# Optimization experiments

Measured on AMD Instinct MI355X. Metric: run time of the kernel, lower is better.

The kernel has to match this reference:

```python
import jax, jax.numpy as jnp
import numpy as np

N = 131072      # number of nodes / samples
IN_DIM = 128    # input_dim
H = 128         # hidden_dim
OUT_DIM = 10    # output_dim


def setup_inputs() -> dict:
    key = jax.random.key(0)
    ks = jax.random.split(key, 20)
    s = 0.05
    def rn(k, shape):
        return jax.random.normal(k, shape, jnp.float32) * s
    return {
        "x": jax.random.normal(ks[0], (N, IN_DIM), jnp.float32),
        # GRU layer 1 (seq_len=1, h0=0 => weight_hh contributes nothing; only b_hh matters)
        "w_ih_f1": rn(ks[1], (3 * H, IN_DIM)), "b_ih_f1": rn(ks[2], (3 * H,)), "b_hh_f1": rn(ks[3], (3 * H,)),
        "w_ih_b1": rn(ks[4], (3 * H, IN_DIM)), "b_ih_b1": rn(ks[5], (3 * H,)), "b_hh_b1": rn(ks[6], (3 * H,)),
        # GRU layer 2 (input 2H)
        "w_ih_f2": rn(ks[7], (3 * H, 2 * H)), "b_ih_f2": rn(ks[8], (3 * H,)), "b_hh_f2": rn(ks[9], (3 * H,)),
        "w_ih_b2": rn(ks[10], (3 * H, 2 * H)), "b_ih_b2": rn(ks[11], (3 * H,)), "b_hh_b2": rn(ks[12], (3 * H,)),
        # GCNConv layers
        "w_g1": rn(ks[13], (2 * H, 128)), "b_g1": rn(ks[14], (128,)),
        "w_g2": rn(ks[15], (128, 64)), "b_g2": rn(ks[16], (64,)),
        # final fc
        "w_fc": rn(ks[17], (64, OUT_DIM)), "b_fc": rn(ks[18], (OUT_DIM,)),
    }


def _gru_cell_zero(x, w_ih, b_ih, b_hh):
    # PyTorch GRU cell with h_prev = 0: h' = (1 - z) * n_gate
    gi = x @ w_ih.T + b_ih                    # [n, 3H]
    ir, iz, inn = jnp.split(gi, 3, axis=-1)
    hr, hz, hn = jnp.split(b_hh, 3)
    r = jax.nn.sigmoid(ir + hr)
    z = jax.nn.sigmoid(iz + hz)
    ng = jnp.tanh(inn + r * hn)
    return (1.0 - z) * ng


def _gcn(x, w, b, sources, targets, n):
    # PyG GCNConv: D^{-1/2}(A+I)D^{-1/2} X W + b, self-loops already in edge lists
    xw = x @ w                                 # [n, out]
    deg = jax.ops.segment_sum(jnp.ones(sources.shape[0], x.dtype), targets, num_segments=n)
    dinv = jax.lax.rsqrt(deg)
    norm = dinv[sources] * dinv[targets]       # [E]
    msg = norm[:, None] * xw[sources]          # gather
    return jax.ops.segment_sum(msg, targets, num_segments=n) + b  # scatter-add


def reference(x, w_ih_f1, b_ih_f1, b_hh_f1, w_ih_b1, b_ih_b1, b_hh_b1,
              w_ih_f2, b_ih_f2, b_hh_f2, w_ih_b2, b_ih_b2, b_hh_b2,
              w_g1, b_g1, w_g2, b_g2, w_fc, b_fc):
    n = x.shape[0]
    # seq_len = 1 => bidirectional GRU output is [fwd_cell(x); bwd_cell(x)]
    h1 = jnp.concatenate([_gru_cell_zero(x, w_ih_f1, b_ih_f1, b_hh_f1),
                          _gru_cell_zero(x, w_ih_b1, b_ih_b1, b_hh_b1)], axis=-1)
    h2 = jnp.concatenate([_gru_cell_zero(h1, w_ih_f2, b_ih_f2, b_hh_f2),
                          _gru_cell_zero(h1, w_ih_b2, b_ih_b2, b_hh_b2)], axis=-1)
    # chain graph, both directions, plus self loops (GCNConv adds them)
    src = jnp.arange(n - 1)
    dst = jnp.arange(1, n)
    ar = jnp.arange(n)
    sources = jnp.concatenate([src, dst, ar])
    targets = jnp.concatenate([dst, src, ar])
    g1 = _gcn(h2, w_g1, b_g1, sources, targets, n)   # dropout is identity in eval
    g2 = _gcn(g1, w_g2, b_g2, sources, targets, n)
    return g2 @ w_fc + b_fc
```

## Files before the change

### kernel.cpp

```cpp
#include <hip/hip_runtime.h>
#include <stdint.h>

#define N_NODES 131072
#define HDIM 128

typedef __bf16 bf16x8 __attribute__((ext_vector_type(8)));
typedef float f32x4 __attribute__((ext_vector_type(4)));
typedef unsigned short ushort_t;

__device__ __forceinline__ ushort_t f2bf(float f) {
    union { float f; uint32_t i; } v; v.f = f;
    uint32_t i = v.i;
    return (ushort_t)((i + 0x7FFFu + ((i >> 16) & 1u)) >> 16);
}

__device__ __forceinline__ void gll16(const ushort_t* g, ushort_t* l) {
    __builtin_amdgcn_global_load_lds(
        (const __attribute__((address_space(1))) uint32_t*)g,
        (__attribute__((address_space(3))) uint32_t*)l, 16, 0, 0);
}

__device__ __forceinline__ bf16x8 ldsw(const ushort_t* base, int R, int g) {
    return *(const bf16x8*)&base[R * 64 + (((g - R) & 7) << 3)];
}

__device__ __forceinline__ float fsig(float x) {
    return __builtin_amdgcn_rcpf(1.0f + __expf(-x));
}
__device__ __forceinline__ float ftanh(float y) {
    float yc = fminf(fmaxf(y, -15.0f), 15.0f);
    float e = __expf(2.0f * yc);
    return (e - 1.0f) * __builtin_amdgcn_rcpf(e + 1.0f);
}

template<int NC>
__device__ __forceinline__ void swz(int b, int& m, int& c) {
    int mhi = b / (8 * NC);
    int rem = b - mhi * (8 * NC);
    c = rem >> 3;
    m = mhi * 8 + (rem & 7);
}

__global__ __launch_bounds__(256) void prep_all(
    const float* __restrict__ w_f1, const float* __restrict__ w_b1,
    const float* __restrict__ w_f2, const float* __restrict__ w_b2,
    ushort_t* __restrict__ PWF1, ushort_t* __restrict__ PWB1,
    ushort_t* __restrict__ PWF2, ushort_t* __restrict__ PWB2,
    const float* __restrict__ w_g1, const float* __restrict__ b_g1,
    const float* __restrict__ w_g2, const float* __restrict__ b_g2,
    const float* __restrict__ w_fc, const float* __restrict__ b_fc,
    ushort_t* __restrict__ M16, float* __restrict__ cc)
{
    __shared__ float wfc_s[640];
    __shared__ float T1[128][10];
    const int t = threadIdx.x;

    if (blockIdx.x < 1152) {
        int idx = blockIdx.x * 256 + t;
        if (idx < 49152) {
            PWF1[idx] = f2bf(w_f1[idx]);
        } else if (idx < 98304) {
            int j = idx - 49152;  PWB1[j] = f2bf(w_b1[j]);
        } else if (idx < 196608) {
            int j = idx - 98304;  PWF2[j] = f2bf(w_f2[j]);
        } else if (idx < 294912) {
            int j = idx - 196608; PWB2[j] = f2bf(w_b2[j]);
        }
        return;
    }

    for (int i = t; i < 640; i += 256) wfc_s[i] = w_fc[i];
    __syncthreads();
    if (t < 128) {
        float s[10];
        #pragma unroll
        for (int j = 0; j < 10; ++j) s[j] = 0.0f;
        const float4* row = (const float4*)(w_g2 + t * 64);
        #pragma unroll
        for (int k4 = 0; k4 < 16; ++k4) {
            float4 v = row[k4];
            #pragma unroll
            for (int j = 0; j < 10; ++j)
                s[j] += v.x * wfc_s[(k4 * 4 + 0) * 10 + j] + v.y * wfc_s[(k4 * 4 + 1) * 10 + j]
                      + v.z * wfc_s[(k4 * 4 + 2) * 10 + j] + v.w * wfc_s[(k4 * 4 + 3) * 10 + j];
        }
        #pragma unroll
        for (int j = 0; j < 10; ++j) T1[t][j] = s[j];
    }
    __syncthreads();
    float m[10];
    #pragma unroll
    for (int j = 0; j < 10; ++j) m[j] = 0.0f;
    const float4* row1 = (const float4*)(w_g1 + t * 128);
    #pragma unroll 4
    for (int k4 = 0; k4 < 32; ++k4) {
        float4 v = row1[k4];
        #pragma unroll
        for (int j = 0; j < 10; ++j)
            m[j] += v.x * T1[k4 * 4 + 0][j] + v.y * T1[k4 * 4 + 1][j]
                  + v.z * T1[k4 * 4 + 2][j] + v.w * T1[k4 * 4 + 3][j];
    }
    #pragma unroll
    for (int j = 0; j < 16; ++j)
        M16[j * 256 + t] = (j < 10) ? f2bf(m[j]) : (ushort_t)0;
    if (t < 10) {
        float s1 = 0.0f;
        for (int k2 = 0; k2 < 128; ++k2) s1 += b_g1[k2] * T1[k2][t];
        cc[t] = s1;
        float s2 = 0.0f;
        for (int k3 = 0; k3 < 64; ++k3) s2 += b_g2[k3] * wfc_s[k3 * 10 + t];
        cc[16 + t] = s2 + b_fc[t];
    }
}

__global__ __launch_bounds__(512, 4) void gru_l1(
    const float* __restrict__ X,
    const ushort_t* __restrict__ Wf,
    const ushort_t* __restrict__ Wb,
    const float* __restrict__ bi_f, const float* __restrict__ bh_f,
    const float* __restrict__ bi_b, const float* __restrict__ bh_b,
    ushort_t* __restrict__ Hout)
{
    __shared__ ushort_t As[2 * 8192];
    __shared__ ushort_t Bs[96 * 64];
    const int tid = threadIdx.x;
    const int m0 = blockIdx.x * 128;
    const int wv = tid >> 6, lane = tid & 63;
    const int lr = lane & 15, lq = lane >> 4;

    #pragma unroll
    for (int p = 0; p < 4; ++p) {
        int ci = p * 512 + tid;
        int reg = ci >> 10, w = ci & 1023, row = w >> 3, slot = w & 7;
        int g = (slot + row) & 7;
        const float* src = X + (size_t)(m0 + row) * 128 + reg * 64 + g * 8;
        float4 f0 = ((const float4*)src)[0];
        float4 f1 = ((const float4*)src)[1];
        bf16x8 t8;
        t8[0] = (__bf16)f0.x; t8[1] = (__bf16)f0.y; t8[2] = (__bf16)f0.z; t8[3] = (__bf16)f0.w;
        t8[4] = (__bf16)f1.x; t8[5] = (__bf16)f1.y; t8[6] = (__bf16)f1.z; t8[7] = (__bf16)f1.w;
        *(bf16x8*)&As[ci * 8] = t8;
    }
    __syncthreads();

    for (int jc = 0; jc < 8; ++jc) {
        const int dir = jc >> 2;
        const int j0 = (jc & 3) * 32;
        const ushort_t* W = dir ? Wb : Wf;
        const float* b_ih = dir ? bi_b : bi_f;
        const float* b_hh = dir ? bh_b : bh_f;
        const int coloff = dir << 7;

        f32x4 acc[3][2];
        #pragma unroll
        for (int g = 0; g < 3; ++g)
            #pragma unroll
            for (int ct = 0; ct < 2; ++ct)
                #pragma unroll
                for (int e = 0; e < 4; ++e) acc[g][ct][e] = 0.0f;

        for (int t = 0; t < 2; ++t) {
            {
                int ci = tid;
                int r96 = ci >> 3, slot = ci & 7, g = (slot + r96) & 7;
                int wr = ((r96 >> 5) << 7) + j0 + (r96 & 31);
                gll16(W + (size_t)wr * 128 + t * 64 + g * 8, &Bs[ci * 8]);
                if (tid < 256) {
                    int ci2 = 512 + tid;
                    int r2 = ci2 >> 3, s2 = ci2 & 7, g2 = (s2 + r2) & 7;
                    int wr2 = ((r2 >> 5) << 7) + j0 + (r2 & 31);
                    gll16(W + (size_t)wr2 * 128 + t * 64 + g2 * 8, &Bs[ci2 * 8]);
                }
            }
            __syncthreads();
            #pragma unroll
            for (int kk = 0; kk < 64; kk += 32) {
                const int g8 = (kk >> 3) + lq;
                bf16x8 a0 = ldsw(&As[t * 8192], wv * 16 + lr, g8);
                #pragma unroll
                for (int g = 0; g < 3; ++g) {
                    #pragma unroll
                    for (int ct = 0; ct < 2; ++ct) {
                        bf16x8 b = ldsw(Bs, g * 32 + ct * 16 + lr, g8);
                        acc[g][ct] = __builtin_amdgcn_mfma_f32_16x16x32_bf16(a0, b, acc[g][ct], 0, 0, 0);
                    }
                }
            }
            __syncthreads();
        }

        #pragma unroll
        for (int ct = 0; ct < 2; ++ct) {
            const int j = j0 + ct * 16 + lr;
            const float br  = b_ih[j] + b_hh[j];
            const float bz  = b_ih[HDIM + j] + b_hh[HDIM + j];
            const float bn  = b_ih[2 * HDIM + j];
            const float bhn = b_hh[2 * HDIM + j];
            #pragma unroll
            for (int r = 0; r < 4; ++r) {
                const int row = m0 + wv * 16 + lq * 4 + r;
                float rg = fsig(acc[0][ct][r] + br);
                float zg = fsig(acc[1][ct][r] + bz);
                float ng = ftanh(acc[2][ct][r] + bn + rg * bhn);
                ((__bf16*)Hout)[(size_t)row * 256 + coloff + j] = (__bf16)((1.0f - zg) * ng);
            }
        }
    }
}

__global__ __launch_bounds__(256, 5) void gru_l2(
    const ushort_t* __restrict__ A,
    const ushort_t* __restrict__ Wf,
    const ushort_t* __restrict__ Wb,
    const float* __restrict__ bi_f, const float* __restrict__ bh_f,
    const float* __restrict__ bi_b, const float* __restrict__ bh_b,
    const ushort_t* __restrict__ M16,
    float* __restrict__ Zp)
{
    __shared__ ushort_t As[128 * 64];
    __shared__ ushort_t Bs[96 * 64];
    const int tid = threadIdx.x;
    int mt, comb;
    swz<8>(blockIdx.x, mt, comb);
    const int m0 = mt * 128;
    const int dir = comb >> 2;
    const int j0 = (comb & 3) * 32;
    const ushort_t* W = dir ? Wb : Wf;
    const float* b_ih = dir ? bi_b : bi_f;
    const float* b_hh = dir ? bh_b : bh_f;
    const int coloff = dir << 7;

    const int wv = tid >> 6, lane = tid & 63;
    const int lr = lane & 15, lq = lane >> 4;
    const int tr = tid >> 3, tc = tid & 7;
    const int sc = ((tr + tc) & 7) << 3;

    f32x4 acc[3][2][2];
    #pragma unroll
    for (int g = 0; g < 3; ++g)
        #pragma unroll
        for (int rt = 0; rt < 2; ++rt)
            #pragma unroll
            for (int ct = 0; ct < 2; ++ct)
                #pragma unroll
                for (int e = 0; e < 4; ++e) acc[g][rt][ct][e] = 0.0f;

    for (int t = 0; t < 4; ++t) {
        const int k0 = t * 64;
        const ushort_t* ga = A + (size_t)(m0 + tr) * 256 + k0 + sc;
        #pragma unroll
        for (int i = 0; i < 4; ++i)
            gll16(ga + (size_t)i * 32 * 256, &As[(i * 256 + tid) * 8]);
        #pragma unroll
        for (int i = 0; i < 3; ++i) {
            int wr = (i << 7) + j0 + tr;
            gll16(W + (size_t)wr * 256 + k0 + sc, &Bs[(i * 256 + tid) * 8]);
        }
        __syncthreads();
        #pragma unroll
        for (int kk = 0; kk < 64; kk += 32) {
            const int g8 = (kk >> 3) + lq;
            bf16x8 a0 = ldsw(As, wv * 32 + lr, g8);
            bf16x8 a1 = ldsw(As, wv * 32 + 16 + lr, g8);
            #pragma unroll
            for (int g = 0; g < 3; ++g) {
                #pragma unroll
                for (int ct = 0; ct < 2; ++ct) {
                    bf16x8 b = ldsw(Bs, g * 32 + ct * 16 + lr, g8);
                    acc[g][0][ct] = __builtin_amdgcn_mfma_f32_16x16x32_bf16(a0, b, acc[g][0][ct], 0, 0, 0);
                    acc[g][1][ct] = __builtin_amdgcn_mfma_f32_16x16x32_bf16(a1, b, acc[g][1][ct], 0, 0, 0);
                }
            }
        }
        __syncthreads();
    }

    const bf16x8 mb = *(const bf16x8*)&M16[lr * 256 + coloff + j0 + lq * 8];

    ushort_t* hs = &As[wv * 1280];
    #pragma unroll
    for (int ct = 0; ct < 2; ++ct) {
        const int j = j0 + ct * 16 + lr;
        const float br  = b_ih[j] + b_hh[j];
        const float bz  = b_ih[HDIM + j] + b_hh[HDIM + j];
        const float bn  = b_ih[2 * HDIM + j];
        const float bhn = b_hh[2 * HDIM + j];
        #pragma unroll
        for (int rt = 0; rt < 2; ++rt) {
            #pragma unroll
            for (int r = 0; r < 4; ++r) {
                const int lrow = rt * 16 + lq * 4 + r;
                float rg = fsig(acc[0][rt][ct][r] + br);
                float zg = fsig(acc[1][rt][ct][r] + bz);
                float ng = ftanh(acc[2][rt][ct][r] + bn + rg * bhn);
                ((__bf16*)hs)[lrow * 40 + ct * 16 + lr] = (__bf16)((1.0f - zg) * ng);
            }
        }
    }
    __syncthreads();

    bf16x8 ha0 = *(const bf16x8*)&hs[lr * 40 + lq * 8];
    bf16x8 ha1 = *(const bf16x8*)&hs[(16 + lr) * 40 + lq * 8];
    f32x4 z0, z1;
    #pragma unroll
    for (int e = 0; e < 4; ++e) { z0[e] = 0.0f; z1[e] = 0.0f; }
    z0 = __builtin_amdgcn_mfma_f32_16x16x32_bf16(ha0, mb, z0, 0, 0, 0);
    z1 = __builtin_amdgcn_mfma_f32_16x16x32_bf16(ha1, mb, z1, 0, 0, 0);

    if (lr < 10) {
        float* zslice = Zp + (size_t)comb * ((size_t)N_NODES * 10);
        #pragma unroll
        for (int r = 0; r < 4; ++r) {
            zslice[(size_t)(m0 + wv * 32 + lq * 4 + r) * 10 + lr] = z0[r];
            zslice[(size_t)(m0 + wv * 32 + 16 + lq * 4 + r) * 10 + lr] = z1[r];
        }
    }
}

__device__ __forceinline__ float dcoef(int i) {
    return (i == 0 || i == N_NODES - 1) ? 0.70710678118654752f : 0.57735026918962576f;
}
__global__ __launch_bounds__(256) void stz(
    const float* __restrict__ Zp, float* __restrict__ out,
    const float* __restrict__ cc)
{
    __shared__ __align__(16) float zl[2600];
    const int tid = threadIdx.x;
    const int n0 = blockIdx.x * 256;
    const bool edge = (blockIdx.x == 0) || (blockIdx.x == gridDim.x - 1);

    if (!edge) {
        const size_t base4 = ((size_t)n0 * 10 - 20) >> 2;
        const float4* Z4 = (const float4*)Zp;
        for (int i4 = tid; i4 < 650; i4 += 256) {
            float4 a = Z4[base4 + i4];
            #pragma unroll
            for (int s = 1; s < 8; ++s) {
                float4 b = Z4[(size_t)s * ((size_t)N_NODES * 10 / 4) + base4 + i4];
                a.x += b.x; a.y += b.y; a.z += b.z; a.w += b.w;
            }
            ((float4*)zl)[i4] = a;
        }
    } else {
        for (int i = tid; i < 2600; i += 256) {
            int nl = i / 10;
            int c = i - nl * 10;
            int n = n0 - 2 + nl;
            float v = 0.0f;
            if (n >= 0 && n < N_NODES) {
                size_t b = (size_t)n * 10 + c;
                #pragma unroll
                for (int s = 0; s < 8; ++s)
                    v += Zp[(size_t)s * ((size_t)N_NODES * 10) + b];
            }
            zl[i] = v;
        }
    }
    __syncthreads();

    const int i = n0 + tid;
    const float d_i = dcoef(i);
    float dsum = d_i;
    if (i - 1 >= 0) dsum += dcoef(i - 1);
    if (i + 1 < N_NODES) dsum += dcoef(i + 1);

    #pragma unroll
    for (int c = 0; c < 10; ++c) {
        float accv = 0.0f;
        #pragma unroll
        for (int oj = -1; oj <= 1; ++oj) {
            int j = i + oj;
            if (j < 0 || j >= N_NODES) continue;
            float dj = dcoef(j);
            float wj = 0.0f;
            #pragma unroll
            for (int ok = -1; ok <= 1; ++ok) {
                int k = j + ok;
                wj += dcoef(k) * zl[(tid + 2 + oj + ok) * 10 + c];
            }
            accv += dj * dj * wj;
        }
        out[(size_t)i * 10 + c] = d_i * accv + d_i * dsum * cc[c] + cc[16 + c];
    }
}

extern "C" void kernel_launch(void* const* d_in, const int* in_sizes, int n_in,
                              void* d_out, int out_size, void* d_ws, size_t ws_size,
                              hipStream_t stream) {
    const float* x     = (const float*)d_in[0];
    const float* w_f1  = (const float*)d_in[1];
    const float* bi_f1 = (const float*)d_in[2];
    const float* bh_f1 = (const float*)d_in[3];
    const float* w_b1  = (const float*)d_in[4];
    const float* bi_b1 = (const float*)d_in[5];
    const float* bh_b1 = (const float*)d_in[6];
    const float* w_f2  = (const float*)d_in[7];
    const float* bi_f2 = (const float*)d_in[8];
    const float* bh_f2 = (const float*)d_in[9];
    const float* w_b2  = (const float*)d_in[10];
    const float* bi_b2 = (const float*)d_in[11];
    const float* bh_b2 = (const float*)d_in[12];
    const float* w_g1  = (const float*)d_in[13];
    const float* b_g1  = (const float*)d_in[14];
    const float* w_g2  = (const float*)d_in[15];
    const float* b_g2  = (const float*)d_in[16];
    const float* w_fc  = (const float*)d_in[17];
    const float* b_fc  = (const float*)d_in[18];

    char* ws = (char*)d_ws;
    ushort_t* h1   = (ushort_t*)(ws);
    float*    Zp   = (float*)(ws + 67108864);
    ushort_t* PWF1 = (ushort_t*)(ws + 134217728);
    ushort_t* PWB1 = PWF1 + 49152;
    ushort_t* PWF2 = PWB1 + 49152;
    ushort_t* PWB2 = PWF2 + 98304;
    ushort_t* M16  = PWB2 + 98304;
    float*    cc   = (float*)(M16 + 4096);

    prep_all<<<1153, 256, 0, stream>>>(w_f1, w_b1, w_f2, w_b2,
                                       PWF1, PWB1, PWF2, PWB2,
                                       w_g1, b_g1, w_g2, b_g2, w_fc, b_fc,
                                       M16, cc);

    gru_l1<<<N_NODES / 128, 512, 0, stream>>>(
        x, PWF1, PWB1, bi_f1, bh_f1, bi_b1, bh_b1, h1);
    gru_l2<<<N_NODES / 128 * 8, 256, 0, stream>>>(
        h1, PWF2, PWB2, bi_f2, bh_f2, bi_b2, bh_b2, M16, Zp);

    stz<<<N_NODES / 256, 256, 0, stream>>>(Zp, (float*)d_out, cc);
}
```

Measured before the change: 277.0 us.

## Keep GRU layer-1 X tile in registers and load full-K weight slabs

The first GRU layer kernel no longer stages the converted X tile in shared memory. Each lane loads and converts its own A fragments straight into registers, which frees 32 KB of LDS. The weight tile now covers the full K=128 in a single load with a 16-slot swizzle, so each column chunk needs two barriers instead of four. Launch bounds ask for 8 blocks per CU to raise occupancy, at the risk of register pressure and spills from the extra fragment registers.

```diff
diff --git a/kernel.cpp b/kernel.cpp
--- a/kernel.cpp
+++ b/kernel.cpp
@@ -22,6 +22,10 @@
 
 __device__ __forceinline__ bf16x8 ldsw(const ushort_t* base, int R, int g) {
     return *(const bf16x8*)&base[R * 64 + (((g - R) & 7) << 3)];
+}
+
+__device__ __forceinline__ bf16x8 ldsw128(const ushort_t* base, int R, int g) {
+    return *(const bf16x8*)&base[R * 128 + (((g - R) & 15) << 3)];
 }
 
 __device__ __forceinline__ float fsig(float x) {
@@ -113,7 +117,7 @@
     }
 }
 
-__global__ __launch_bounds__(512, 4) void gru_l1(
+__global__ __launch_bounds__(512, 8) void gru_l1(
     const float* __restrict__ X,
     const ushort_t* __restrict__ Wf,
     const ushort_t* __restrict__ Wb,
@@ -121,27 +125,27 @@
     const float* __restrict__ bi_b, const float* __restrict__ bh_b,
     ushort_t* __restrict__ Hout)
 {
-    __shared__ ushort_t As[2 * 8192];
-    __shared__ ushort_t Bs[96 * 64];
+    __shared__ ushort_t Bs[96 * 128];
     const int tid = threadIdx.x;
     const int m0 = blockIdx.x * 128;
     const int wv = tid >> 6, lane = tid & 63;
     const int lr = lane & 15, lq = lane >> 4;
 
-    #pragma unroll
-    for (int p = 0; p < 4; ++p) {
-        int ci = p * 512 + tid;
-        int reg = ci >> 10, w = ci & 1023, row = w >> 3, slot = w & 7;
-        int g = (slot + row) & 7;
-        const float* src = X + (size_t)(m0 + row) * 128 + reg * 64 + g * 8;
-        float4 f0 = ((const float4*)src)[0];
-        float4 f1 = ((const float4*)src)[1];
-        bf16x8 t8;
-        t8[0] = (__bf16)f0.x; t8[1] = (__bf16)f0.y; t8[2] = (__bf16)f0.z; t8[3] = (__bf16)f0.w;
-        t8[4] = (__bf16)f1.x; t8[5] = (__bf16)f1.y; t8[6] = (__bf16)f1.z; t8[7] = (__bf16)f1.w;
-        *(bf16x8*)&As[ci * 8] = t8;
-    }
-    __syncthreads();
+    bf16x8 af[4];
+    {
+        const float* xr = X + (size_t)(m0 + wv * 16 + lr) * 128 + lq * 8;
+        #pragma unroll
+        for (int c = 0; c < 4; ++c) {
+            float4 f0 = ((const float4*)(xr + c * 32))[0];
+            float4 f1 = ((const float4*)(xr + c * 32))[1];
+            bf16x8 t8;
+            t8[0] = (__bf16)f0.x; t8[1] = (__bf16)f0.y;
+            t8[2] = (__bf16)f0.z; t8[3] = (__bf16)f0.w;
+            t8[4] = (__bf16)f1.x; t8[5] = (__bf16)f1.y;
+            t8[6] = (__bf16)f1.z; t8[7] = (__bf16)f1.w;
+            af[c] = t8;
+        }
+    }
 
     for (int jc = 0; jc < 8; ++jc) {
         const int dir = jc >> 2;
@@ -151,6 +155,16 @@
         const float* b_hh = dir ? bh_b : bh_f;
         const int coloff = dir << 7;
 
+        #pragma unroll
+        for (int p = 0; p < 3; ++p) {
+            int ci = p * 512 + tid;
+            int r96 = ci >> 4, slot = ci & 15;
+            int g16 = (slot + r96) & 15;
+            int wr = ((r96 >> 5) << 7) + j0 + (r96 & 31);
+            gll16(W + (size_t)wr * 128 + g16 * 8, &Bs[ci * 8]);
+        }
+        __syncthreads();
+
         f32x4 acc[3][2];
         #pragma unroll
         for (int g = 0; g < 3; ++g)
@@ -159,34 +173,16 @@
                 #pragma unroll
                 for (int e = 0; e < 4; ++e) acc[g][ct][e] = 0.0f;
 
-        for (int t = 0; t < 2; ++t) {
-            {
-                int ci = tid;
-                int r96 = ci >> 3, slot = ci & 7, g = (slot + r96) & 7;
-                int wr = ((r96 >> 5) << 7) + j0 + (r96 & 31);
-                gll16(W + (size_t)wr * 128 + t * 64 + g * 8, &Bs[ci * 8]);
-                if (tid < 256) {
-                    int ci2 = 512 + tid;
-                    int r2 = ci2 >> 3, s2 = ci2 & 7, g2 = (s2 + r2) & 7;
-                    int wr2 = ((r2 >> 5) << 7) + j0 + (r2 & 31);
-                    gll16(W + (size_t)wr2 * 128 + t * 64 + g2 * 8, &Bs[ci2 * 8]);
+        #pragma unroll
+        for (int c = 0; c < 4; ++c) {
+            #pragma unroll
+            for (int g = 0; g < 3; ++g) {
+                #pragma unroll
+                for (int ct = 0; ct < 2; ++ct) {
+                    bf16x8 b = ldsw128(Bs, g * 32 + ct * 16 + lr, c * 4 + lq);
+                    acc[g][ct] = __builtin_amdgcn_mfma_f32_16x16x32_bf16(af[c], b, acc[g][ct], 0, 0, 0);
                 }
             }
-            __syncthreads();
-            #pragma unroll
-            for (int kk = 0; kk < 64; kk += 32) {
-                const int g8 = (kk >> 3) + lq;
-                bf16x8 a0 = ldsw(&As[t * 8192], wv * 16 + lr, g8);
-                #pragma unroll
-                for (int g = 0; g < 3; ++g) {
-                    #pragma unroll
-                    for (int ct = 0; ct < 2; ++ct) {
-                        bf16x8 b = ldsw(Bs, g * 32 + ct * 16 + lr, g8);
-                        acc[g][ct] = __builtin_amdgcn_mfma_f32_16x16x32_bf16(a0, b, acc[g][ct], 0, 0, 0);
-                    }
-                }
-            }
-            __syncthreads();
         }
 
         #pragma unroll
@@ -205,6 +201,7 @@
                 ((__bf16*)Hout)[(size_t)row * 256 + coloff + j] = (__bf16)((1.0f - zg) * ng);
             }
         }
+        __syncthreads();
     }
 }
 
```

Result: slower. 310.4 us (+12.1%).
